# Kernel optimization log

Hardware: AMD Instinct MI355X
Metric: run time of the kernel (lower is better)

## Reference

```python
import jax, jax.numpy as jnp
import numpy as np

B, T, C, I, E, K, V, H = 4, 512, 512, 2048, 32, 2, 32000, 8
D = C // H
EPS = 1e-5


def setup_inputs() -> dict:
    key = jax.random.key(0)
    ks = jax.random.split(key, 16)
    s = 0.02
    inp = {
        "input_ids": jax.random.randint(ks[0], (B, T), 0, V),
        "emb": jax.random.normal(ks[1], (V, C), jnp.float32) * s,
        "wq": jax.random.normal(ks[2], (C, C), jnp.float32) * s,
        "wk": jax.random.normal(ks[3], (C, C), jnp.float32) * s,
        "wv": jax.random.normal(ks[4], (C, C), jnp.float32) * s,
        "wo": jax.random.normal(ks[5], (C, C), jnp.float32) * s,
        "gate": jax.random.normal(ks[6], (C, E), jnp.float32) * s,
        "w1": jax.random.normal(ks[7], (E, C, I), jnp.float32) * s,
        "w2": jax.random.normal(ks[8], (E, I, C), jnp.float32) * s,
        "g1": jnp.ones((C,), jnp.float32) + jax.random.normal(ks[9], (C,), jnp.float32) * 0.01,
        "b1": jax.random.normal(ks[10], (C,), jnp.float32) * 0.01,
        "g2": jnp.ones((C,), jnp.float32) + jax.random.normal(ks[11], (C,), jnp.float32) * 0.01,
        "b2": jax.random.normal(ks[12], (C,), jnp.float32) * 0.01,
        "lm_head": jax.random.normal(ks[13], (C, V), jnp.float32) * s,
    }
    return inp


def _ln(x, g, b):
    mu = jnp.mean(x, axis=-1, keepdims=True)
    var = jnp.mean(jnp.square(x - mu), axis=-1, keepdims=True)
    return (x - mu) * jax.lax.rsqrt(var + EPS) * g + b


def reference(input_ids, emb, wq, wk, wv, wo, gate, w1, w2, g1, b1, g2, b2, lm_head):
    h = emb[input_ids]  # [B,T,C]
    # --- attention block ---
    x = _ln(h, g1, b1)
    q = (x @ wq).reshape(B, T, H, D).transpose(0, 2, 1, 3)  # [B,H,T,D]
    k = (x @ wk).reshape(B, T, H, D).transpose(0, 2, 1, 3)
    v = (x @ wv).reshape(B, T, H, D).transpose(0, 2, 1, 3)
    scores = jnp.einsum('bhqd,bhkd->bhqk', q, k) / jnp.sqrt(jnp.float32(D))
    causal = jnp.tril(jnp.ones((T, T), bool))
    scores = jnp.where(causal, scores, jnp.finfo(scores.dtype).min)
    attn = jax.nn.softmax(scores, axis=-1)
    ao = jnp.einsum('bhqk,bhkd->bhqd', attn, v)
    ao = ao.transpose(0, 2, 1, 3).reshape(B, T, C) @ wo
    h = h + ao
    # --- MoE block ---
    x2 = _ln(h, g2, b2)          # hidden_states_for_moe [B,T,C]
    flat = x2.reshape(-1, C)     # [N,C], N = B*T tokens
    router_logits = flat @ gate  # [N,E]
    rw, sel = jax.lax.top_k(router_logits, K)   # [N,K]
    rw = jax.nn.softmax(rw.astype(jnp.float32), axis=-1)
    # dense per-expert FFN, then mask to selected experts (same math as
    # torch's loop: unselected (token,expert) slots stay zero)
    hidden = jax.nn.gelu(jnp.einsum('tc,eci->tei', flat, w1), approximate=False)
    all_out = jnp.einsum('tei,eic->tec', hidden, w2)  # [N,E,C]
    sel_mask = jnp.sum(jax.nn.one_hot(sel, E, dtype=all_out.dtype), axis=1)  # [N,E]
    full_expert_outputs = all_out * sel_mask[:, :, None]
    gathered = jnp.take_along_axis(full_expert_outputs, sel[:, :, None], axis=1)  # [N,K,C]
    moe_out = jnp.einsum('tk,tkc->tc', rw, gathered).reshape(B, T, C)
    h = h + moe_out
    logits = h @ lm_head
    return logits, full_expert_outputs, router_logits, x2
```

## Files before the change

### kernel.cpp

```cpp
#include <hip/hip_runtime.h>
#include <hip/hip_bf16.h>

#define BATCH 4
#define SEQ   512
#define CH    512
#define NTOK  2048
#define FF    2048
#define NEXP  32
#define TOPK  2
#define VOCAB 32000
#define NHEAD 8
#define HDIM  64
#define EPSF  1e-5f

typedef __attribute__((ext_vector_type(8))) short short8v;
typedef __attribute__((ext_vector_type(4))) float f32x4;

__device__ __forceinline__ unsigned short bf16r(float f) {
  unsigned int u = __float_as_uint(f);
  u = (u + 0x7FFFu + ((u >> 16) & 1u)) >> 16;
  return (unsigned short)u;
}

__device__ __forceinline__ float block_reduce_sum(float v, float* sbuf) {
  #pragma unroll
  for (int off = 32; off > 0; off >>= 1) v += __shfl_down(v, off, 64);
  const int lane = threadIdx.x & 63, wid = threadIdx.x >> 6;
  __syncthreads();
  if (lane == 0) sbuf[wid] = v;
  __syncthreads();
  return sbuf[0] + sbuf[1] + sbuf[2] + sbuf[3];
}

__device__ __forceinline__ float gelu_exact(float v) {
  return 0.5f * v * (1.f + erff(v * 0.70710678118654752f));
}

__global__ __launch_bounds__(256) void transpose_cvt_kernel(
    const float* __restrict__ in, unsigned short* __restrict__ out, int R, int C) {
  __shared__ float T[64][65];
  const size_t zoff = (size_t)blockIdx.z * R * C;
  in += zoff; out += zoff;
  const int r0 = blockIdx.y << 6;
  const int c0 = blockIdx.x << 6;
  const int t = threadIdx.x;
  const int lr = t >> 4;
  const int lc = (t & 15) << 2;
  #pragma unroll
  for (int rr = 0; rr < 64; rr += 16) {
    const float4 v = *(const float4*)(in + (size_t)(r0 + lr + rr) * C + c0 + lc);
    T[lr + rr][lc + 0] = v.x; T[lr + rr][lc + 1] = v.y;
    T[lr + rr][lc + 2] = v.z; T[lr + rr][lc + 3] = v.w;
  }
  __syncthreads();
  const int oc = t >> 2;
  const int rs = (t & 3) << 4;
  unsigned int pk[8];
  #pragma unroll
  for (int j = 0; j < 8; ++j) {
    const float a = T[rs + 2 * j][oc];
    const float b = T[rs + 2 * j + 1][oc];
    pk[j] = (unsigned int)bf16r(a) | ((unsigned int)bf16r(b) << 16);
  }
  unsigned short* op = out + (size_t)(c0 + oc) * R + r0 + rs;
  *(uint4*)(op)     = make_uint4(pk[0], pk[1], pk[2], pk[3]);
  *(uint4*)(op + 8) = make_uint4(pk[4], pk[5], pk[6], pk[7]);
}

__global__ __launch_bounds__(256) void embed_ln_kernel(
    const int* __restrict__ ids, const float* __restrict__ emb,
    const float* __restrict__ g, const float* __restrict__ b,
    float* __restrict__ h, float* __restrict__ x) {
  __shared__ float sbuf[4];
  const int n = blockIdx.x, t = threadIdx.x;
  const float2 v = *(const float2*)(emb + (size_t)ids[n] * CH + 2 * t);
  *(float2*)(h + (size_t)n * CH + 2 * t) = v;
  const float mu = block_reduce_sum(v.x + v.y, sbuf) * (1.f / CH);
  const float d0 = v.x - mu, d1 = v.y - mu;
  const float var = block_reduce_sum(d0 * d0 + d1 * d1, sbuf) * (1.f / CH);
  const float rstd = rsqrtf(var + EPSF);
  const float2 gg = *(const float2*)(g + 2 * t);
  const float2 bb = *(const float2*)(b + 2 * t);
  *(float2*)(x + (size_t)n * CH + 2 * t) =
      make_float2(d0 * rstd * gg.x + bb.x, d1 * rstd * gg.y + bb.y);
}

__global__ __launch_bounds__(256) void ln2_kernel(
    const float* __restrict__ in, const float* __restrict__ g,
    const float* __restrict__ b, float* __restrict__ outf,
    unsigned short* __restrict__ outbf) {
  __shared__ float sbuf[4];
  const int n = blockIdx.x, t = threadIdx.x;
  const float2 v = *(const float2*)(in + (size_t)n * CH + 2 * t);
  const float mu = block_reduce_sum(v.x + v.y, sbuf) * (1.f / CH);
  const float d0 = v.x - mu, d1 = v.y - mu;
  const float var = block_reduce_sum(d0 * d0 + d1 * d1, sbuf) * (1.f / CH);
  const float rstd = rsqrtf(var + EPSF);
  const float2 gg = *(const float2*)(g + 2 * t);
  const float2 bb = *(const float2*)(b + 2 * t);
  const float o0 = d0 * rstd * gg.x + bb.x;
  const float o1 = d1 * rstd * gg.y + bb.y;
  *(float2*)(outf + (size_t)n * CH + 2 * t) = make_float2(o0, o1);
  ((unsigned int*)outbf)[(size_t)n * (CH / 2) + t] =
      (unsigned int)bf16r(o0) | ((unsigned int)bf16r(o1) << 16);
}

__global__ __launch_bounds__(256) void gemm_f32_kernel(
    const float* __restrict__ A, const float* __restrict__ B,
    const float* __restrict__ Res, float* __restrict__ C,
    int M, int N, int K) {
  __shared__ float As[32][68];
  __shared__ float Bs[32][132];
  const int m0 = blockIdx.y << 6;
  const int n0 = blockIdx.x << 7;
  const int t  = threadIdx.x;
  const int tm = t >> 4;
  const int tn = t & 15;
  float acc[4][8];
  #pragma unroll
  for (int i = 0; i < 4; ++i)
    #pragma unroll
    for (int j = 0; j < 8; ++j) acc[i][j] = 0.f;

  const int ar = t >> 3;
  const int ac = (t & 7) << 2;
  const int bk = t >> 3;
  const int bn = (t & 7) << 4;

  for (int kt = 0; kt < K; kt += 32) {
    #pragma unroll
    for (int rr = 0; rr < 64; rr += 32) {
      float4 a = *(const float4*)(A + (size_t)(m0 + ar + rr) * K + kt + ac);
      As[ac + 0][ar + rr] = a.x; As[ac + 1][ar + rr] = a.y;
      As[ac + 2][ar + rr] = a.z; As[ac + 3][ar + rr] = a.w;
    }
    const float* bp = B + (size_t)(kt + bk) * N + n0 + bn;
    #pragma unroll
    for (int j = 0; j < 16; j += 4)
      *(float4*)&Bs[bk][bn + j] = *(const float4*)(bp + j);
    __syncthreads();
    #pragma unroll
    for (int k = 0; k < 32; ++k) {
      const float4 av = *(const float4*)&As[k][tm << 2];
      const float4 bl = *(const float4*)&Bs[k][tn << 2];
      const float4 bh = *(const float4*)&Bs[k][64 + (tn << 2)];
      const float a_[4] = {av.x, av.y, av.z, av.w};
      const float b_[8] = {bl.x, bl.y, bl.z, bl.w, bh.x, bh.y, bh.z, bh.w};
      #pragma unroll
      for (int i = 0; i < 4; ++i)
        #pragma unroll
        for (int j = 0; j < 8; ++j)
          acc[i][j] = fmaf(a_[i], b_[j], acc[i][j]);
    }
    __syncthreads();
  }
  #pragma unroll
  for (int i = 0; i < 4; ++i) {
    const int row = m0 + (tm << 2) + i;
    float* cp = C + (size_t)row * N + n0 + (tn << 2);
    float4 lo = make_float4(acc[i][0], acc[i][1], acc[i][2], acc[i][3]);
    float4 hi = make_float4(acc[i][4], acc[i][5], acc[i][6], acc[i][7]);
    if (Res) {
      const float* rp = Res + (size_t)row * N + n0 + (tn << 2);
      const float4 r0 = *(const float4*)rp;
      const float4 r1 = *(const float4*)(rp + 64);
      lo.x += r0.x; lo.y += r0.y; lo.z += r0.z; lo.w += r0.w;
      hi.x += r1.x; hi.y += r1.y; hi.z += r1.z; hi.w += r1.w;
    }
    *(float4*)cp        = lo;
    *(float4*)(cp + 64) = hi;
  }
}

template <int SWZ>
__global__ __launch_bounds__(256) void gemm_bf16_kernel(
    const unsigned short* __restrict__ A, const unsigned short* __restrict__ BT,
    float* __restrict__ C, int M, int N, int K) {
  int bx = blockIdx.x, by = blockIdx.y;
  if (SWZ) {
    const int gx = gridDim.x;
    const int nb = gx * gridDim.y;
    int bid = by * gx + bx;
    bid = (bid & 7) * (nb >> 3) + (bid >> 3);
    bx = bid % gx;
    by = bid / gx;
  }
  __shared__ unsigned short As[128][72];
  __shared__ unsigned short Bs[128][72];
  const int m0 = by << 7;
  const int n0 = bx << 7;
  const int t  = threadIdx.x;
  const int w  = t >> 6;
  const int l  = t & 63;
  const int wm = (w >> 1) << 6;
  const int wn = (w & 1) << 6;
  const int fr = l & 15;
  const int fg = l >> 4;
  f32x4 acc[4][4];
  #pragma unroll
  for (int i = 0; i < 4; ++i)
    #pragma unroll
    for (int j = 0; j < 4; ++j) acc[i][j] = (f32x4){0.f, 0.f, 0.f, 0.f};

  const int sr = t >> 1;
  const int sc = (t & 1) << 5;
  const unsigned short* ap = A  + (size_t)(m0 + sr) * K + sc;
  const unsigned short* bp = BT + (size_t)(n0 + sr) * K + sc;

  for (int kt = 0; kt < K; kt += 64) {
    #pragma unroll
    for (int j = 0; j < 4; ++j) {
      *(uint4*)&As[sr][sc + (j << 3)] = *(const uint4*)(ap + kt + (j << 3));
      *(uint4*)&Bs[sr][sc + (j << 3)] = *(const uint4*)(bp + kt + (j << 3));
    }
    __syncthreads();
    #pragma unroll
    for (int kk = 0; kk < 64; kk += 32) {
      short8v afr[4], bfr[4];
      #pragma unroll
      for (int i = 0; i < 4; ++i)
        afr[i] = *(const short8v*)&As[wm + (i << 4) + fr][kk + (fg << 3)];
      #pragma unroll
      for (int j = 0; j < 4; ++j)
        bfr[j] = *(const short8v*)&Bs[wn + (j << 4) + fr][kk + (fg << 3)];
      #pragma unroll
      for (int i = 0; i < 4; ++i)
        #pragma unroll
        for (int j = 0; j < 4; ++j)
          acc[i][j] = __builtin_amdgcn_mfma_f32_16x16x32_bf16(afr[i], bfr[j], acc[i][j], 0, 0, 0);
    }
    __syncthreads();
  }
  #pragma unroll
  for (int i = 0; i < 4; ++i) {
    #pragma unroll
    for (int j = 0; j < 4; ++j) {
      const int col = n0 + wn + (j << 4) + fr;
      const int rowb = m0 + wm + (i << 4) + (fg << 2);
      #pragma unroll
      for (int r = 0; r < 4; ++r)
        C[(size_t)(rowb + r) * N + col] = acc[i][j][r];
    }
  }
}

__global__ __launch_bounds__(256) void attn_kernel(
    const float* __restrict__ q, const float* __restrict__ kbuf,
    const float* __restrict__ vbuf, float* __restrict__ ao) {
  __shared__ float Ks[64][68];
  __shared__ float Vs[64][68];
  __shared__ float Sx[64][65];
  const int bh = blockIdx.x;
  const int qt = blockIdx.y;
  const int b  = bh >> 3;
  const int hh = bh & 7;
  const int t  = threadIdx.x;
  const int qi   = t >> 2;
  const int part = t & 3;
  const int qglob = (qt << 6) + qi;
  const size_t qoff = (size_t)(b * SEQ + qglob) * CH + hh * HDIM + (part << 4);
  float qreg[16];
  #pragma unroll
  for (int j = 0; j < 16; j += 4) {
    const float4 v4 = *(const float4*)(q + qoff + j);
    qreg[j] = v4.x; qreg[j + 1] = v4.y; qreg[j + 2] = v4.z; qreg[j + 3] = v4.w;
  }
  float o[16];
  #pragma unroll
  for (int j = 0; j < 16; ++j) o[j] = 0.f;
  float m = -3.0e38f, l = 0.f;
  const int lr = t >> 2;
  const int lc = (t & 3) << 4;
  for (int kt = 0; kt <= qt; ++kt) {
    const size_t base = (size_t)(b * SEQ + (kt << 6) + lr) * CH + hh * HDIM + lc;
    #pragma unroll
    for (int j = 0; j < 16; j += 4) {
      *(float4*)&Ks[lr][lc + j] = *(const float4*)(kbuf + base + j);
      *(float4*)&Vs[lr][lc + j] = *(const float4*)(vbuf + base + j);
    }
    __syncthreads();
    float sloc[16];
    float tmax = -3.0e38f;
    for (int kk = 0; kk < 64; ++kk) {
      float p = 0.f;
      const float* kr = &Ks[kk][part << 4];
      #pragma unroll
      for (int j = 0; j < 16; ++j) p = fmaf(qreg[j], kr[j], p);
      p += __shfl_xor(p, 1, 64);
      p += __shfl_xor(p, 2, 64);
      p *= 0.125f;
      if (((kt << 6) + kk) > qglob) p = -3.0e38f;
      tmax = fmaxf(tmax, p);
      if ((kk & 3) == part) sloc[kk >> 2] = p;
    }
    const float mnew = fmaxf(m, tmax);
    const float corr = expf(m - mnew);
    float lsum = 0.f;
    #pragma unroll
    for (int j = 0; j < 16; ++j) {
      const float pe = expf(sloc[j] - mnew);
      lsum += pe;
      Sx[qi][(j << 2) + part] = pe;
    }
    lsum += __shfl_xor(lsum, 1, 64);
    lsum += __shfl_xor(lsum, 2, 64);
    l = l * corr + lsum;
    m = mnew;
    #pragma unroll
    for (int j = 0; j < 16; ++j) o[j] *= corr;
    __syncthreads();
    for (int kk = 0; kk < 64; ++kk) {
      const float pv = Sx[qi][kk];
      const float* vr = &Vs[kk][part << 4];
      #pragma unroll
      for (int j = 0; j < 16; ++j) o[j] = fmaf(pv, vr[j], o[j]);
    }
    __syncthreads();
  }
  const float inv = 1.f / l;
  #pragma unroll
  for (int j = 0; j < 16; j += 4)
    *(float4*)(ao + qoff + j) =
        make_float4(o[j] * inv, o[j + 1] * inv, o[j + 2] * inv, o[j + 3] * inv);
}

__global__ __launch_bounds__(256) void router_kernel(
    const float* __restrict__ x2, const float* __restrict__ gate,
    float* __restrict__ rl, float* __restrict__ rw, int* __restrict__ sel,
    int* __restrict__ counts, int* __restrict__ lists) {
  __shared__ float xrow[CH];
  __shared__ float lg[NEXP];
  const int n = blockIdx.x;
  const int t = threadIdx.x;
  xrow[t]       = x2[(size_t)n * CH + t];
  xrow[t + 256] = x2[(size_t)n * CH + t + 256];
  __syncthreads();
  const int e = t >> 3, i = t & 7;
  float p = 0.f;
  const float* gp = gate + e;
  for (int c = i * 64; c < i * 64 + 64; ++c) p = fmaf(xrow[c], gp[(size_t)c * NEXP], p);
  p += __shfl_xor(p, 1, 64);
  p += __shfl_xor(p, 2, 64);
  p += __shfl_xor(p, 4, 64);
  if (i == 0) { lg[e] = p; rl[(size_t)n * NEXP + e] = p; }
  __syncthreads();
  if (t == 0) {
    int i0 = 0; float v0 = lg[0];
    for (int j = 1; j < NEXP; ++j) if (lg[j] > v0) { v0 = lg[j]; i0 = j; }
    int i1 = (i0 == 0) ? 1 : 0; float v1 = lg[i1];
    for (int j = 0; j < NEXP; ++j) {
      if (j == i0 || j == i1) continue;
      if (lg[j] > v1) { v1 = lg[j]; i1 = j; }
    }
    const float ex = expf(v1 - v0);
    const float den = 1.f + ex;
    rw[n * 2]     = 1.f / den;
    rw[n * 2 + 1] = ex / den;
    sel[n * 2]     = i0;
    sel[n * 2 + 1] = i1;
    const int s0 = atomicAdd(&counts[i0], 1);
    lists[i0 * NTOK + s0] = n * 2;
    const int s1 = atomicAdd(&counts[i1], 1);
    lists[i1 * NTOK + s1] = n * 2 + 1;
  }
}

__global__ __launch_bounds__(256) void moe_fc1_bf16(
    const unsigned short* __restrict__ x2bf, const unsigned short* __restrict__ w1T,
    const int* __restrict__ counts, const int* __restrict__ lists,
    unsigned short* __restrict__ hidden) {
  const int e  = blockIdx.y;
  const int nt = counts[e];
  const int mt = blockIdx.z << 6;
  if (mt >= nt) return;
  const int i0 = blockIdx.x << 7;
  __shared__ unsigned short As[64][72];
  __shared__ unsigned short Bs[128][72];
  __shared__ int ls[64];
  const int* lst = lists + e * NTOK;
  const int t = threadIdx.x;
  if (t < 64) ls[t] = (mt + t < nt) ? lst[mt + t] : -1;
  __syncthreads();
  const int w  = t >> 6, l = t & 63;
  const int wm = (w >> 1) << 5;
  const int wn = (w & 1) << 6;
  const int fr = l & 15, fg = l >> 4;
  f32x4 acc[2][4];
  #pragma unroll
  for (int i = 0; i < 2; ++i)
    #pragma unroll
    for (int j = 0; j < 4; ++j) acc[i][j] = (f32x4){0.f, 0.f, 0.f, 0.f};

  const int arow = t >> 2, akc = (t & 3) << 4;
  const int brow = t >> 1, bkc = (t & 1) << 5;
  const int apid = ls[arow];
  const unsigned short* arp = (apid >= 0) ? (x2bf + (size_t)(apid >> 1) * CH) : nullptr;
  const unsigned short* brp = w1T + (size_t)e * FF * CH + (size_t)(i0 + brow) * CH;

  for (int kt = 0; kt < CH; kt += 64) {
    if (arp) {
      *(uint4*)&As[arow][akc + 0] = *(const uint4*)(arp + kt + akc + 0);
      *(uint4*)&As[arow][akc + 8] = *(const uint4*)(arp + kt + akc + 8);
    } else {
      *(uint4*)&As[arow][akc + 0] = make_uint4(0, 0, 0, 0);
      *(uint4*)&As[arow][akc + 8] = make_uint4(0, 0, 0, 0);
    }
    #pragma unroll
    for (int j = 0; j < 4; ++j)
      *(uint4*)&Bs[brow][bkc + (j << 3)] = *(const uint4*)(brp + kt + bkc + (j << 3));
    __syncthreads();
    #pragma unroll
    for (int kk = 0; kk < 64; kk += 32) {
      short8v afr[2], bfr[4];
      #pragma unroll
      for (int i = 0; i < 2; ++i)
        afr[i] = *(const short8v*)&As[wm + (i << 4) + fr][kk + (fg << 3)];
      #pragma unroll
      for (int j = 0; j < 4; ++j)
        bfr[j] = *(const short8v*)&Bs[wn + (j << 4) + fr][kk + (fg << 3)];
      #pragma unroll
      for (int i = 0; i < 2; ++i)
        #pragma unroll
        for (int j = 0; j < 4; ++j)
          acc[i][j] = __builtin_amdgcn_mfma_f32_16x16x32_bf16(afr[i], bfr[j], acc[i][j], 0, 0, 0);
    }
    __syncthreads();
  }
  #pragma unroll
  for (int i = 0; i < 2; ++i) {
    #pragma unroll
    for (int r = 0; r < 4; ++r) {
      const int lrow = wm + (i << 4) + (fg << 2) + r;
      const int pid = ls[lrow];
      if (pid < 0) continue;
      unsigned short* hp = hidden + (size_t)pid * FF + i0 + wn + fr;
      #pragma unroll
      for (int j = 0; j < 4; ++j)
        hp[j << 4] = bf16r(gelu_exact(acc[i][j][r]));
    }
  }
}

__global__ __launch_bounds__(256) void moe_fc2_bf16(
    const unsigned short* __restrict__ hidden, const unsigned short* __restrict__ w2T,
    const int* __restrict__ counts, const int* __restrict__ lists,
    float* __restrict__ fe) {
  const int e  = blockIdx.y;
  const int nt = counts[e];
  const int mt = blockIdx.z << 6;
  if (mt >= nt) return;
  const int c0 = blockIdx.x << 7;
  __shared__ unsigned short As[64][72];
  __shared__ unsigned short Bs[128][72];
  __shared__ int ls[64];
  const int* lst = lists + e * NTOK;
  const int t = threadIdx.x;
  if (t < 64) ls[t] = (mt + t < nt) ? lst[mt + t] : -1;
  __syncthreads();
  const int w  = t >> 6, l = t & 63;
  const int wm = (w >> 1) << 5;
  const int wn = (w & 1) << 6;
  const int fr = l & 15, fg = l >> 4;
  f32x4 acc[2][4];
  #pragma unroll
  for (int i = 0; i < 2; ++i)
    #pragma unroll
    for (int j = 0; j < 4; ++j) acc[i][j] = (f32x4){0.f, 0.f, 0.f, 0.f};

  const int arow = t >> 2, akc = (t & 3) << 4;
  const int brow = t >> 1, bkc = (t & 1) << 5;
  const int apid = ls[arow];
  const unsigned short* arp = (apid >= 0) ? (hidden + (size_t)apid * FF) : nullptr;
  const unsigned short* brp = w2T + (size_t)e * CH * FF + (size_t)(c0 + brow) * FF;

  for (int kt = 0; kt < FF; kt += 64) {
    if (arp) {
      *(uint4*)&As[arow][akc + 0] = *(const uint4*)(arp + kt + akc + 0);
      *(uint4*)&As[arow][akc + 8] = *(const uint4*)(arp + kt + akc + 8);
    } else {
      *(uint4*)&As[arow][akc + 0] = make_uint4(0, 0, 0, 0);
      *(uint4*)&As[arow][akc + 8] = make_uint4(0, 0, 0, 0);
    }
    #pragma unroll
    for (int j = 0; j < 4; ++j)
      *(uint4*)&Bs[brow][bkc + (j << 3)] = *(const uint4*)(brp + kt + bkc + (j << 3));
    __syncthreads();
    #pragma unroll
    for (int kk = 0; kk < 64; kk += 32) {
      short8v afr[2], bfr[4];
      #pragma unroll
      for (int i = 0; i < 2; ++i)
        afr[i] = *(const short8v*)&As[wm + (i << 4) + fr][kk + (fg << 3)];
      #pragma unroll
      for (int j = 0; j < 4; ++j)
        bfr[j] = *(const short8v*)&Bs[wn + (j << 4) + fr][kk + (fg << 3)];
      #pragma unroll
      for (int i = 0; i < 2; ++i)
        #pragma unroll
        for (int j = 0; j < 4; ++j)
          acc[i][j] = __builtin_amdgcn_mfma_f32_16x16x32_bf16(afr[i], bfr[j], acc[i][j], 0, 0, 0);
    }
    __syncthreads();
  }
  #pragma unroll
  for (int i = 0; i < 2; ++i) {
    #pragma unroll
    for (int r = 0; r < 4; ++r) {
      const int lrow = wm + (i << 4) + (fg << 2) + r;
      const int pid = ls[lrow];
      if (pid < 0) continue;
      const int n = pid >> 1;
      float* op = fe + ((size_t)n * NEXP + e) * CH + c0 + wn + fr;
      #pragma unroll
      for (int j = 0; j < 4; ++j)
        op[j << 4] = acc[i][j][r];
    }
  }
}

__global__ __launch_bounds__(256) void combine_kernel(
    const float* __restrict__ h2, const float* __restrict__ fe,
    const float* __restrict__ rw, const int* __restrict__ sel,
    unsigned short* __restrict__ hfbf) {
  const int idx = blockIdx.x * 256 + threadIdx.x;
  const int n = idx >> 7;
  const int c = (idx & 127) << 2;
  const float w0 = rw[n * 2], w1 = rw[n * 2 + 1];
  const int s0 = sel[n * 2], s1 = sel[n * 2 + 1];
  const float* base = fe + (size_t)n * NEXP * CH + c;
  const float4 f0 = *(const float4*)(base + (size_t)s0 * CH);
  const float4 f1 = *(const float4*)(base + (size_t)s1 * CH);
  const float4 a  = *(const float4*)(h2 + (size_t)n * CH + c);
  const float ox = a.x + w0 * f0.x + w1 * f1.x;
  const float oy = a.y + w0 * f0.y + w1 * f1.y;
  const float oz = a.z + w0 * f0.z + w1 * f1.z;
  const float ow = a.w + w0 * f0.w + w1 * f1.w;
  uint2 pk;
  pk.x = (unsigned int)bf16r(ox) | ((unsigned int)bf16r(oy) << 16);
  pk.y = (unsigned int)bf16r(oz) | ((unsigned int)bf16r(ow) << 16);
  *(uint2*)(hfbf + (size_t)n * CH + c) = pk;
}

extern "C" void kernel_launch(void* const* d_in, const int* in_sizes, int n_in,
                              void* d_out, int out_size, void* d_ws, size_t ws_size,
                              hipStream_t stream) {
  const int*   ids  = (const int*)d_in[0];
  const float* emb  = (const float*)d_in[1];
  const float* wq   = (const float*)d_in[2];
  const float* wk   = (const float*)d_in[3];
  const float* wv   = (const float*)d_in[4];
  const float* wo   = (const float*)d_in[5];
  const float* gate = (const float*)d_in[6];
  const float* w1   = (const float*)d_in[7];
  const float* w2   = (const float*)d_in[8];
  const float* g1   = (const float*)d_in[9];
  const float* b1   = (const float*)d_in[10];
  const float* g2   = (const float*)d_in[11];
  const float* b2   = (const float*)d_in[12];
  const float* lmh  = (const float*)d_in[13];

  float* out        = (float*)d_out;
  float* out_logits = out;
  float* out_fe     = out_logits + (size_t)NTOK * VOCAB;
  float* out_rl     = out_fe + (size_t)NTOK * NEXP * CH;
  float* out_x2     = out_rl + (size_t)NTOK * NEXP;

  unsigned short* w1T    = (unsigned short*)(out_logits);
  unsigned short* w2T    = (unsigned short*)(out_logits + 16777216);
  unsigned short* hidden = (unsigned short*)(out_logits + 33554432);
  float*          x      = out_logits + 37748736;
  float*          qb     = out_logits + 38797312;
  float*          kb     = out_logits + 39845888;
  float*          vb     = out_logits + 40894464;
  float*          ao     = out_logits + 41943040;
  float*          h      = out_logits + 42991616;
  float*          h2     = out_logits + 44040192;
  unsigned short* x2_bf  = (unsigned short*)(out_logits + 45088768);

  float* ws    = (float*)d_ws;
  unsigned short* lmhT  = (unsigned short*)ws;
  unsigned short* hf_bf = (unsigned short*)(ws + 8192000);
  float* rw    = ws + 8716288;
  int*   sel   = (int*)(rw + NTOK * TOPK);
  int*   counts= sel + NTOK * TOPK;
  int*   lists = counts + 64;

  hipMemsetAsync(counts, 0, NEXP * sizeof(int), stream);
  hipMemsetAsync(out_fe, 0, (size_t)NTOK * NEXP * CH * sizeof(float), stream);

  transpose_cvt_kernel<<<dim3(500, 8, 1),   256, 0, stream>>>(lmh, lmhT, CH, VOCAB);
  transpose_cvt_kernel<<<dim3(32, 8, NEXP), 256, 0, stream>>>(w1, w1T, CH, FF);
  transpose_cvt_kernel<<<dim3(8, 32, NEXP), 256, 0, stream>>>(w2, w2T, FF, CH);

  embed_ln_kernel<<<NTOK, 256, 0, stream>>>(ids, emb, g1, b1, h, x);

  gemm_f32_kernel<<<dim3(CH / 128, NTOK / 64), 256, 0, stream>>>(x, wq, nullptr, qb, NTOK, CH, CH);
  gemm_f32_kernel<<<dim3(CH / 128, NTOK / 64), 256, 0, stream>>>(x, wk, nullptr, kb, NTOK, CH, CH);
  gemm_f32_kernel<<<dim3(CH / 128, NTOK / 64), 256, 0, stream>>>(x, wv, nullptr, vb, NTOK, CH, CH);

  attn_kernel<<<dim3(BATCH * NHEAD, SEQ / 64), 256, 0, stream>>>(qb, kb, vb, ao);

  gemm_f32_kernel<<<dim3(CH / 128, NTOK / 64), 256, 0, stream>>>(ao, wo, h, h2, NTOK, CH, CH);

  ln2_kernel<<<NTOK, 256, 0, stream>>>(h2, g2, b2, out_x2, x2_bf);

  router_kernel<<<NTOK, 256, 0, stream>>>(out_x2, gate, out_rl, rw, sel, counts, lists);

  moe_fc1_bf16<<<dim3(FF / 128, NEXP, NTOK / 64), 256, 0, stream>>>(x2_bf, w1T, counts, lists, hidden);
  moe_fc2_bf16<<<dim3(CH / 128, NEXP, NTOK / 64), 256, 0, stream>>>(hidden, w2T, counts, lists, out_fe);

  combine_kernel<<<dim3(NTOK * CH / 1024), 256, 0, stream>>>(h2, out_fe, rw, sel, hf_bf);

  gemm_bf16_kernel<1><<<dim3(VOCAB / 128, NTOK / 128), 256, 0, stream>>>(
      hf_bf, lmhT, out_logits, NTOK, VOCAB, CH);
}
```

Measured before the change: 1.263 ms.

## Load GEMM B tiles directly into LDS and fuse QKV projections into one launch

Replaces register-staged global-to-LDS copies in the bf16 lm_head GEMM and both MoE expert GEMMs with global_load_lds 16-byte direct transfers, which requires dropping the LDS row padding. It also merges the three Q/K/V fp32 projection launches into one grid using blockIdx.z to select the weight. The aim is to cut VGPR traffic and load instructions plus launch overhead, at the risk of LDS bank conflicts on the MFMA fragment reads now that the padding is gone.

```diff
diff --git a/kernel.cpp b/kernel.cpp
--- a/kernel.cpp
+++ b/kernel.cpp
@@ -15,6 +15,10 @@
 
 typedef __attribute__((ext_vector_type(8))) short short8v;
 typedef __attribute__((ext_vector_type(4))) float f32x4;
+
+#define GLD16(g, lds) __builtin_amdgcn_global_load_lds(                      \
+    (const __attribute__((address_space(1))) void*)(g),                      \
+    (__attribute__((address_space(3))) void*)(lds), 16, 0, 0)
 
 __device__ __forceinline__ unsigned short bf16r(float f) {
   unsigned int u = __float_as_uint(f);
@@ -105,6 +109,68 @@
       (unsigned int)bf16r(o0) | ((unsigned int)bf16r(o1) << 16);
 }
 
+__global__ __launch_bounds__(256) void gemm_f32_qkv_kernel(
+    const float* __restrict__ A,
+    const float* __restrict__ Wq, const float* __restrict__ Wk,
+    const float* __restrict__ Wv,
+    float* __restrict__ Oq, float* __restrict__ Ok, float* __restrict__ Ov,
+    int M, int N, int K) {
+  const float* B = (blockIdx.z == 0) ? Wq : (blockIdx.z == 1) ? Wk : Wv;
+  float*       C = (blockIdx.z == 0) ? Oq : (blockIdx.z == 1) ? Ok : Ov;
+  __shared__ float As[32][68];
+  __shared__ float Bs[32][132];
+  const int m0 = blockIdx.y << 6;
+  const int n0 = blockIdx.x << 7;
+  const int t  = threadIdx.x;
+  const int tm = t >> 4;
+  const int tn = t & 15;
+  float acc[4][8];
+  #pragma unroll
+  for (int i = 0; i < 4; ++i)
+    #pragma unroll
+    for (int j = 0; j < 8; ++j) acc[i][j] = 0.f;
+
+  const int ar = t >> 3;
+  const int ac = (t & 7) << 2;
+  const int bk = t >> 3;
+  const int bn = (t & 7) << 4;
+
+  for (int kt = 0; kt < K; kt += 32) {
+    #pragma unroll
+    for (int rr = 0; rr < 64; rr += 32) {
+      float4 a = *(const float4*)(A + (size_t)(m0 + ar + rr) * K + kt + ac);
+      As[ac + 0][ar + rr] = a.x; As[ac + 1][ar + rr] = a.y;
+      As[ac + 2][ar + rr] = a.z; As[ac + 3][ar + rr] = a.w;
+    }
+    const float* bp = B + (size_t)(kt + bk) * N + n0 + bn;
+    #pragma unroll
+    for (int j = 0; j < 16; j += 4)
+      *(float4*)&Bs[bk][bn + j] = *(const float4*)(bp + j);
+    __syncthreads();
+    #pragma unroll
+    for (int k = 0; k < 32; ++k) {
+      const float4 av = *(const float4*)&As[k][tm << 2];
+      const float4 bl = *(const float4*)&Bs[k][tn << 2];
+      const float4 bh = *(const float4*)&Bs[k][64 + (tn << 2)];
+      const float a_[4] = {av.x, av.y, av.z, av.w};
+      const float b_[8] = {bl.x, bl.y, bl.z, bl.w, bh.x, bh.y, bh.z, bh.w};
+      #pragma unroll
+      for (int i = 0; i < 4; ++i)
+        #pragma unroll
+        for (int j = 0; j < 8; ++j)
+          acc[i][j] = fmaf(a_[i], b_[j], acc[i][j]);
+    }
+    __syncthreads();
+  }
+  #pragma unroll
+  for (int i = 0; i < 4; ++i) {
+    const int row = m0 + (tm << 2) + i;
+    float* cp = C + (size_t)row * N + n0 + (tn << 2);
+    *(float4*)cp        = make_float4(acc[i][0], acc[i][1], acc[i][2], acc[i][3]);
+    *(float4*)(cp + 64) = make_float4(acc[i][4], acc[i][5], acc[i][6], acc[i][7]);
+  }
+}
+
 __global__ __launch_bounds__(256) void gemm_f32_kernel(
     const float* __restrict__ A, const float* __restrict__ B,
     const float* __restrict__ Res, float* __restrict__ C,
@@ -185,8 +251,8 @@
     bx = bid % gx;
     by = bid / gx;
   }
-  __shared__ unsigned short As[128][72];
-  __shared__ unsigned short Bs[128][72];
+  __shared__ unsigned short As[128][64];
+  __shared__ unsigned short Bs[128][64];
   const int m0 = by << 7;
   const int n0 = bx << 7;
   const int t  = threadIdx.x;
@@ -196,22 +262,20 @@
   const int wn = (w & 1) << 6;
   const int fr = l & 15;
   const int fg = l >> 4;
+  const int lrow = l >> 3;
+  const int lcol = (l & 7) << 3;
   f32x4 acc[4][4];
   #pragma unroll
   for (int i = 0; i < 4; ++i)
     #pragma unroll
     for (int j = 0; j < 4; ++j) acc[i][j] = (f32x4){0.f, 0.f, 0.f, 0.f};
 
-  const int sr = t >> 1;
-  const int sc = (t & 1) << 5;
-  const unsigned short* ap = A  + (size_t)(m0 + sr) * K + sc;
-  const unsigned short* bp = BT + (size_t)(n0 + sr) * K + sc;
-
   for (int kt = 0; kt < K; kt += 64) {
     #pragma unroll
-    for (int j = 0; j < 4; ++j) {
-      *(uint4*)&As[sr][sc + (j << 3)] = *(const uint4*)(ap + kt + (j << 3));
-      *(uint4*)&Bs[sr][sc + (j << 3)] = *(const uint4*)(bp + kt + (j << 3));
+    for (int q = 0; q < 4; ++q) {
+      const int r = (w << 5) + (q << 3);
+      GLD16(A  + (size_t)(m0 + r + lrow) * K + kt + lcol, &As[r][0]);
+      GLD16(BT + (size_t)(n0 + r + lrow) * K + kt + lcol, &Bs[r][0]);
     }
     __syncthreads();
     #pragma unroll
@@ -375,7 +439,7 @@
   if (mt >= nt) return;
   const int i0 = blockIdx.x << 7;
   __shared__ unsigned short As[64][72];
-  __shared__ unsigned short Bs[128][72];
+  __shared__ unsigned short Bs[128][64];
   __shared__ int ls[64];
   const int* lst = lists + e * NTOK;
   const int t = threadIdx.x;
@@ -385,6 +449,7 @@
   const int wm = (w >> 1) << 5;
   const int wn = (w & 1) << 6;
   const int fr = l & 15, fg = l >> 4;
+  const int lrow = l >> 3, lcol = (l & 7) << 3;
   f32x4 acc[2][4];
   #pragma unroll
   for (int i = 0; i < 2; ++i)
@@ -392,10 +457,9 @@
     for (int j = 0; j < 4; ++j) acc[i][j] = (f32x4){0.f, 0.f, 0.f, 0.f};
 
   const int arow = t >> 2, akc = (t & 3) << 4;
-  const int brow = t >> 1, bkc = (t & 1) << 5;
   const int apid = ls[arow];
   const unsigned short* arp = (apid >= 0) ? (x2bf + (size_t)(apid >> 1) * CH) : nullptr;
-  const unsigned short* brp = w1T + (size_t)e * FF * CH + (size_t)(i0 + brow) * CH;
+  const unsigned short* w1e = w1T + (size_t)e * FF * CH;
 
   for (int kt = 0; kt < CH; kt += 64) {
     if (arp) {
@@ -406,8 +470,10 @@
       *(uint4*)&As[arow][akc + 8] = make_uint4(0, 0, 0, 0);
     }
     #pragma unroll
-    for (int j = 0; j < 4; ++j)
-      *(uint4*)&Bs[brow][bkc + (j << 3)] = *(const uint4*)(brp + kt + bkc + (j << 3));
+    for (int q = 0; q < 4; ++q) {
+      const int r = (w << 5) + (q << 3);
+      GLD16(w1e + (size_t)(i0 + r + lrow) * CH + kt + lcol, &Bs[r][0]);
+    }
     __syncthreads();
     #pragma unroll
     for (int kk = 0; kk < 64; kk += 32) {
@@ -430,8 +496,8 @@
   for (int i = 0; i < 2; ++i) {
     #pragma unroll
     for (int r = 0; r < 4; ++r) {
-      const int lrow = wm + (i << 4) + (fg << 2) + r;
-      const int pid = ls[lrow];
+      const int lrow2 = wm + (i << 4) + (fg << 2) + r;
+      const int pid = ls[lrow2];
       if (pid < 0) continue;
       unsigned short* hp = hidden + (size_t)pid * FF + i0 + wn + fr;
       #pragma unroll
@@ -451,7 +517,7 @@
   if (mt >= nt) return;
   const int c0 = blockIdx.x << 7;
   __shared__ unsigned short As[64][72];
-  __shared__ unsigned short Bs[128][72];
+  __shared__ unsigned short Bs[128][64];
   __shared__ int ls[64];
   const int* lst = lists + e * NTOK;
   const int t = threadIdx.x;
@@ -461,6 +527,7 @@
   const int wm = (w >> 1) << 5;
   const int wn = (w & 1) << 6;
   const int fr = l & 15, fg = l >> 4;
+  const int lrow = l >> 3, lcol = (l & 7) << 3;
   f32x4 acc[2][4];
   #pragma unroll
   for (int i = 0; i < 2; ++i)
@@ -468,10 +535,9 @@
     for (int j = 0; j < 4; ++j) acc[i][j] = (f32x4){0.f, 0.f, 0.f, 0.f};
 
   const int arow = t >> 2, akc = (t & 3) << 4;
-  const int brow = t >> 1, bkc = (t & 1) << 5;
   const int apid = ls[arow];
   const unsigned short* arp = (apid >= 0) ? (hidden + (size_t)apid * FF) : nullptr;
-  const unsigned short* brp = w2T + (size_t)e * CH * FF + (size_t)(c0 + brow) * FF;
+  const unsigned short* w2e = w2T + (size_t)e * CH * FF;
 
   for (int kt = 0; kt < FF; kt += 64) {
     if (arp) {
@@ -482,8 +548,10 @@
       *(uint4*)&As[arow][akc + 8] = make_uint4(0, 0, 0, 0);
     }
     #pragma unroll
-    for (int j = 0; j < 4; ++j)
-      *(uint4*)&Bs[brow][bkc + (j << 3)] = *(const uint4*)(brp + kt + bkc + (j << 3));
+    for (int q = 0; q < 4; ++q) {
+      const int r = (w << 5) + (q << 3);
+      GLD16(w2e + (size_t)(c0 + r + lrow) * FF + kt + lcol, &Bs[r][0]);
+    }
     __syncthreads();
     #pragma unroll
     for (int kk = 0; kk < 64; kk += 32) {
@@ -506,8 +574,8 @@
   for (int i = 0; i < 2; ++i) {
     #pragma unroll
     for (int r = 0; r < 4; ++r) {
-      const int lrow = wm + (i << 4) + (fg << 2) + r;
-      const int pid = ls[lrow];
+      const int lrow2 = wm + (i << 4) + (fg << 2) + r;
+      const int pid = ls[lrow2];
       if (pid < 0) continue;
       const int n = pid >> 1;
       float* op = fe + ((size_t)n * NEXP + e) * CH + c0 + wn + fr;
@@ -594,9 +662,8 @@
 
   embed_ln_kernel<<<NTOK, 256, 0, stream>>>(ids, emb, g1, b1, h, x);
 
-  gemm_f32_kernel<<<dim3(CH / 128, NTOK / 64), 256, 0, stream>>>(x, wq, nullptr, qb, NTOK, CH, CH);
-  gemm_f32_kernel<<<dim3(CH / 128, NTOK / 64), 256, 0, stream>>>(x, wk, nullptr, kb, NTOK, CH, CH);
-  gemm_f32_kernel<<<dim3(CH / 128, NTOK / 64), 256, 0, stream>>>(x, wv, nullptr, vb, NTOK, CH, CH);
+  gemm_f32_qkv_kernel<<<dim3(CH / 128, NTOK / 64, 3), 256, 0, stream>>>(
+      x, wq, wk, wv, qb, kb, vb, NTOK, CH, CH);
 
   attn_kernel<<<dim3(BATCH * NHEAD, SEQ / 64), 256, 0, stream>>>(qb, kb, vb, ao);
 
```

Measured after the change: 1.178 ms. 6.8% less time.
